# Kernel optimization log

Measured on AMD Instinct MI355X. Metric: run time of the kernel, lower is better.

## Reference

```python
import jax, jax.numpy as jnp
import numpy as np

EPS = 1e-3  # Keras BatchNormalization default epsilon
K = 7

def _bn(x, gamma, beta, mean, var):
    return gamma * (x - mean) * jax.lax.rsqrt(var + EPS) + beta

def setup_inputs() -> dict:
    key = jax.random.key(0)
    ks = jax.random.split(key, 4)
    B, L, Cin, F = 64, 512, 64, 128
    out_len = L - K + 1
    return {
        "x": jax.random.normal(ks[0], (B, L, Cin), jnp.float32),
        "conv_w": jax.random.normal(ks[1], (K, Cin, F), jnp.float32) * (1.0 / np.sqrt(K * Cin)),
        "conv_b": jnp.zeros((F,), jnp.float32),
        "bn1_gamma": jnp.ones((F,), jnp.float32),
        "bn1_beta": jnp.zeros((F,), jnp.float32),
        "bn1_mean": jnp.zeros((F,), jnp.float32),
        "bn1_var": jnp.ones((F,), jnp.float32),
        "local_w": jax.random.normal(ks[2], (out_len, K * F, F), jnp.float32) * (1.0 / np.sqrt(K * F)),
        "local_b": jnp.zeros((out_len, F), jnp.float32),
        "bn2_gamma": jnp.ones((F,), jnp.float32),
        "bn2_beta": jnp.zeros((F,), jnp.float32),
        "bn2_mean": jnp.zeros((F,), jnp.float32),
        "bn2_var": jnp.ones((F,), jnp.float32),
    }

def reference(x, conv_w, conv_b, bn1_gamma, bn1_beta, bn1_mean, bn1_var,
              local_w, local_b, bn2_gamma, bn2_beta, bn2_mean, bn2_var):
    # Conv1D, padding='same'  (NWC / WIO)
    y = jax.lax.conv_general_dilated(
        x, conv_w, window_strides=(1,), padding="SAME",
        dimension_numbers=("NWC", "WIO", "NWC")) + conv_b
    y = jax.nn.relu(_bn(y, bn1_gamma, bn1_beta, bn1_mean, bn1_var))

    # LocallyConnected1D, padding='valid': per-position unshared weights
    B, L, F = y.shape
    out_len = L - K + 1
    idx = jnp.arange(out_len)[:, None] + jnp.arange(K)[None, :]  # (out_len, K)
    patches = y[:, idx, :].reshape(B, out_len, K * F)             # (B, out_len, K*F)
    z = jnp.einsum("blk,lkf->blf", patches, local_w) + local_b    # (B, out_len, F)
    z = jax.nn.relu(_bn(z, bn2_gamma, bn2_beta, bn2_mean, bn2_var))
    return z
```

## Files before the change

### kernel.cpp

```cpp
#include <hip/hip_runtime.h>
#include <hip/hip_bf16.h>

typedef __attribute__((ext_vector_type(8))) short bf16x8;
typedef __attribute__((ext_vector_type(4))) float f32x4;

#define BB   64
#define LL   512
#define CIN  64
#define FF   128
#define KW   7
#define OUTL 506
#define LPAD 518
#define KC   448
#define KL   896
#define EPSV 1e-3f

static __device__ __forceinline__ short f2bf(float f) {
    unsigned u = __builtin_bit_cast(unsigned, f);
    unsigned r = (u + 0x7fffu + ((u >> 16) & 1u)) >> 16;
    return (short)r;
}

__global__ void pad_cvt_kernel(const float* __restrict__ x, short* __restrict__ xp) {
    int i = blockIdx.x * 256 + threadIdx.x;
    if (i >= BB * LPAD * CIN) return;
    int c  = i & (CIN - 1);
    int t  = i >> 6;
    int lp = t % LPAD;
    int b  = t / LPAD;
    float v = 0.0f;
    int l = lp - 3;
    if (l >= 0 && l < LL) v = x[(b * LL + l) * CIN + c];
    xp[i] = f2bf(v);
}

__global__ __launch_bounds__(256) void conv_bn_kernel(
    const short* __restrict__ xp, const float* __restrict__ w,
    const float* __restrict__ cb, const float* __restrict__ g,
    const float* __restrict__ be, const float* __restrict__ mu,
    const float* __restrict__ va, short* __restrict__ y) {
    const int lane = threadIdx.x & 63;
    const int wid  = threadIdx.x >> 6;
    const int m0   = blockIdx.x * 64;
    const int nb   = wid * 32;
    const int q    = lane >> 4;
    const int ln   = lane & 15;

    const short* arow[4];
#pragma unroll
    for (int mt = 0; mt < 4; ++mt) {
        int m = m0 + mt * 16 + ln;
        int b = m >> 9, l = m & 511;
        arow[mt] = xp + (b * LPAD + l) * CIN;
    }

    f32x4 acc[4][2];
#pragma unroll
    for (int mt = 0; mt < 4; ++mt)
#pragma unroll
        for (int nt = 0; nt < 2; ++nt) acc[mt][nt] = (f32x4){0.f, 0.f, 0.f, 0.f};

#pragma unroll 2
    for (int kc = 0; kc < KC; kc += 32) {
        const int ko = kc + q * 8;
        bf16x8 a[4];
#pragma unroll
        for (int mt = 0; mt < 4; ++mt)
            a[mt] = *(const bf16x8*)(arow[mt] + ko);
        bf16x8 bf[2];
#pragma unroll
        for (int nt = 0; nt < 2; ++nt) {
            const int n = nb + nt * 16 + ln;
            const float* wp = w + (size_t)ko * FF + n;
#pragma unroll
            for (int j = 0; j < 8; ++j) bf[nt][j] = f2bf(wp[(size_t)j * FF]);
        }
#pragma unroll
        for (int mt = 0; mt < 4; ++mt)
#pragma unroll
            for (int nt = 0; nt < 2; ++nt)
                acc[mt][nt] = __builtin_amdgcn_mfma_f32_16x16x32_bf16(
                    a[mt], bf[nt], acc[mt][nt], 0, 0, 0);
    }

#pragma unroll
    for (int nt = 0; nt < 2; ++nt) {
        const int n = nb + nt * 16 + ln;
        const float s  = g[n] * rsqrtf(va[n] + EPSV);
        const float b2 = s * (cb[n] - mu[n]) + be[n];
#pragma unroll
        for (int mt = 0; mt < 4; ++mt) {
            const int mbase = m0 + mt * 16 + q * 4;
#pragma unroll
            for (int r = 0; r < 4; ++r) {
                float v = fmaxf(acc[mt][nt][r] * s + b2, 0.0f);
                y[(size_t)(mbase + r) * FF + n] = f2bf(v);
            }
        }
    }
}

__global__ __launch_bounds__(256) void local_bn_kernel(
    const short* __restrict__ y, const float* __restrict__ lw,
    const float* __restrict__ lb, const float* __restrict__ g,
    const float* __restrict__ be, const float* __restrict__ mu,
    const float* __restrict__ va, float* __restrict__ out) {
    const int l    = blockIdx.x;
    const int lane = threadIdx.x & 63;
    const int wid  = threadIdx.x >> 6;
    const int nb   = wid * 32;
    const int q    = lane >> 4;
    const int ln   = lane & 15;

    const short* arow[4];
#pragma unroll
    for (int mt = 0; mt < 4; ++mt) {
        const int b = mt * 16 + ln;
        arow[mt] = y + (size_t)b * (LL * FF) + (size_t)l * FF;
    }
    const float* wl = lw + (size_t)l * (KL * FF);

    f32x4 acc[4][2];
#pragma unroll
    for (int mt = 0; mt < 4; ++mt)
#pragma unroll
        for (int nt = 0; nt < 2; ++nt) acc[mt][nt] = (f32x4){0.f, 0.f, 0.f, 0.f};

#pragma unroll 2
    for (int kc = 0; kc < KL; kc += 32) {
        const int ko = kc + q * 8;
        bf16x8 a[4];
#pragma unroll
        for (int mt = 0; mt < 4; ++mt)
            a[mt] = *(const bf16x8*)(arow[mt] + ko);
        bf16x8 bf[2];
#pragma unroll
        for (int nt = 0; nt < 2; ++nt) {
            const int n = nb + nt * 16 + ln;
            const float* wp = wl + (size_t)ko * FF + n;
#pragma unroll
            for (int j = 0; j < 8; ++j) bf[nt][j] = f2bf(wp[(size_t)j * FF]);
        }
#pragma unroll
        for (int mt = 0; mt < 4; ++mt)
#pragma unroll
            for (int nt = 0; nt < 2; ++nt)
                acc[mt][nt] = __builtin_amdgcn_mfma_f32_16x16x32_bf16(
                    a[mt], bf[nt], acc[mt][nt], 0, 0, 0);
    }

#pragma unroll
    for (int nt = 0; nt < 2; ++nt) {
        const int n = nb + nt * 16 + ln;
        const float s  = g[n] * rsqrtf(va[n] + EPSV);
        const float b2 = s * (lb[(size_t)l * FF + n] - mu[n]) + be[n];
#pragma unroll
        for (int mt = 0; mt < 4; ++mt) {
            const int bbase = mt * 16 + q * 4;
#pragma unroll
            for (int r = 0; r < 4; ++r) {
                float v = fmaxf(acc[mt][nt][r] * s + b2, 0.0f);
                out[(size_t)(bbase + r) * (OUTL * FF) + (size_t)l * FF + n] = v;
            }
        }
    }
}

extern "C" void kernel_launch(void* const* d_in, const int* in_sizes, int n_in,
                              void* d_out, int out_size, void* d_ws, size_t ws_size,
                              hipStream_t stream) {
    const float* x       = (const float*)d_in[0];
    const float* conv_w  = (const float*)d_in[1];
    const float* conv_b  = (const float*)d_in[2];
    const float* bn1_g   = (const float*)d_in[3];
    const float* bn1_b   = (const float*)d_in[4];
    const float* bn1_m   = (const float*)d_in[5];
    const float* bn1_v   = (const float*)d_in[6];
    const float* local_w = (const float*)d_in[7];
    const float* local_b = (const float*)d_in[8];
    const float* bn2_g   = (const float*)d_in[9];
    const float* bn2_b   = (const float*)d_in[10];
    const float* bn2_m   = (const float*)d_in[11];
    const float* bn2_v   = (const float*)d_in[12];
    float* out = (float*)d_out;

    short* xp  = (short*)d_ws;
    short* ybf = xp + (size_t)BB * LPAD * CIN;

    const int npad = BB * LPAD * CIN;
    pad_cvt_kernel<<<(npad + 255) / 256, 256, 0, stream>>>(x, xp);
    conv_bn_kernel<<<(BB * LL) / 64, 256, 0, stream>>>(
        xp, conv_w, conv_b, bn1_g, bn1_b, bn1_m, bn1_v, ybf);
    local_bn_kernel<<<OUTL, 256, 0, stream>>>(
        ybf, local_w, local_b, bn2_g, bn2_b, bn2_m, bn2_v, out);
}
```

Before: 379.4 us.

## Pre-transpose conv weights to bf16 and stage local weights through double-buffered LDS

The prep kernel now also converts the conv weights to bf16 in an N-major layout, so the conv kernel loads B fragments as single 16-byte vectors instead of eight strided fp32 loads each. The locally connected kernel streams each position's fp32 weight chunk into a double-buffered LDS tile with direct global-to-LDS loads, overlapping the next chunk's fetch with the current chunk's MFMAs. Fragments are then gathered from LDS with strided reads and converted to bf16. This adds one barrier per chunk, 32KB of LDS per block, and extra workspace for the transposed weights.

```diff
diff --git a/kernel.cpp b/kernel.cpp
--- a/kernel.cpp
+++ b/kernel.cpp
@@ -13,7 +13,14 @@
 #define LPAD 518
 #define KC   448
 #define KL   896
+#define BK   32
+#define NCH  28
 #define EPSV 1e-3f
+
+#define NPAD  (BB * LPAD * CIN)
+#define PADB  (NPAD / 256)
+#define NWT   (FF * KC)
+#define WTB   (NWT / 256)
 
 static __device__ __forceinline__ short f2bf(float f) {
     unsigned u = __builtin_bit_cast(unsigned, f);
@@ -21,21 +28,34 @@
     return (short)r;
 }
 
-__global__ void pad_cvt_kernel(const float* __restrict__ x, short* __restrict__ xp) {
-    int i = blockIdx.x * 256 + threadIdx.x;
-    if (i >= BB * LPAD * CIN) return;
-    int c  = i & (CIN - 1);
-    int t  = i >> 6;
-    int lp = t % LPAD;
-    int b  = t / LPAD;
-    float v = 0.0f;
-    int l = lp - 3;
-    if (l >= 0 && l < LL) v = x[(b * LL + l) * CIN + c];
-    xp[i] = f2bf(v);
+static __device__ __forceinline__ void g2lds16(const float* g, float* l) {
+    __builtin_amdgcn_global_load_lds(
+        (const __attribute__((address_space(1))) unsigned int*)g,
+        (__attribute__((address_space(3))) unsigned int*)l, 16, 0, 0);
+}
+
+__global__ void prep_kernel(const float* __restrict__ x, const float* __restrict__ w,
+                            short* __restrict__ xp, short* __restrict__ wt) {
+    if (blockIdx.x < PADB) {
+        int i = blockIdx.x * 256 + threadIdx.x;
+        int c  = i & (CIN - 1);
+        int t  = i >> 6;
+        int lp = t % LPAD;
+        int b  = t / LPAD;
+        float v = 0.0f;
+        int l = lp - 3;
+        if (l >= 0 && l < LL) v = x[(b * LL + l) * CIN + c];
+        xp[i] = f2bf(v);
+    } else {
+        int i = (blockIdx.x - PADB) * 256 + threadIdx.x;
+        int n = i / KC;
+        int k = i - n * KC;
+        wt[i] = f2bf(w[(size_t)k * FF + n]);
+    }
 }
 
 __global__ __launch_bounds__(256) void conv_bn_kernel(
-    const short* __restrict__ xp, const float* __restrict__ w,
+    const short* __restrict__ xp, const short* __restrict__ wt,
     const float* __restrict__ cb, const float* __restrict__ g,
     const float* __restrict__ be, const float* __restrict__ mu,
     const float* __restrict__ va, short* __restrict__ y) {
@@ -53,6 +73,10 @@
         int b = m >> 9, l = m & 511;
         arow[mt] = xp + (b * LPAD + l) * CIN;
     }
+    const short* brow[2];
+#pragma unroll
+    for (int nt = 0; nt < 2; ++nt)
+        brow[nt] = wt + (size_t)(nb + nt * 16 + ln) * KC;
 
     f32x4 acc[4][2];
 #pragma unroll
@@ -63,18 +87,11 @@
 #pragma unroll 2
     for (int kc = 0; kc < KC; kc += 32) {
         const int ko = kc + q * 8;
-        bf16x8 a[4];
-#pragma unroll
-        for (int mt = 0; mt < 4; ++mt)
-            a[mt] = *(const bf16x8*)(arow[mt] + ko);
-        bf16x8 bf[2];
-#pragma unroll
-        for (int nt = 0; nt < 2; ++nt) {
-            const int n = nb + nt * 16 + ln;
-            const float* wp = w + (size_t)ko * FF + n;
-#pragma unroll
-            for (int j = 0; j < 8; ++j) bf[nt][j] = f2bf(wp[(size_t)j * FF]);
-        }
+        bf16x8 a[4], bf[2];
+#pragma unroll
+        for (int mt = 0; mt < 4; ++mt) a[mt] = *(const bf16x8*)(arow[mt] + ko);
+#pragma unroll
+        for (int nt = 0; nt < 2; ++nt) bf[nt] = *(const bf16x8*)(brow[nt] + ko);
 #pragma unroll
         for (int mt = 0; mt < 4; ++mt)
 #pragma unroll
@@ -105,6 +122,7 @@
     const float* __restrict__ lb, const float* __restrict__ g,
     const float* __restrict__ be, const float* __restrict__ mu,
     const float* __restrict__ va, float* __restrict__ out) {
+    __shared__ float wtile[2][BK * FF];
     const int l    = blockIdx.x;
     const int lane = threadIdx.x & 63;
     const int wid  = threadIdx.x >> 6;
@@ -112,13 +130,12 @@
     const int q    = lane >> 4;
     const int ln   = lane & 15;
 
+    const float* wl = lw + (size_t)l * (KL * FF);
+
     const short* arow[4];
 #pragma unroll
-    for (int mt = 0; mt < 4; ++mt) {
-        const int b = mt * 16 + ln;
-        arow[mt] = y + (size_t)b * (LL * FF) + (size_t)l * FF;
-    }
-    const float* wl = lw + (size_t)l * (KL * FF);
+    for (int mt = 0; mt < 4; ++mt)
+        arow[mt] = y + (size_t)(mt * 16 + ln) * (LL * FF) + (size_t)l * FF;
 
     f32x4 acc[4][2];
 #pragma unroll
@@ -126,20 +143,38 @@
 #pragma unroll
         for (int nt = 0; nt < 2; ++nt) acc[mt][nt] = (f32x4){0.f, 0.f, 0.f, 0.f};
 
-#pragma unroll 2
-    for (int kc = 0; kc < KL; kc += 32) {
-        const int ko = kc + q * 8;
+    {
+        const float* src = wl;
+#pragma unroll
+        for (int r = 0; r < 4; ++r)
+            g2lds16(src + (size_t)(r * 256 + wid * 64 + lane) * 4,
+                    &wtile[0][(r * 256 + wid * 64) * 4]);
+    }
+
+    for (int c = 0; c < NCH; ++c) {
+        __syncthreads();
+        if (c + 1 < NCH) {
+            const float* src = wl + (size_t)(c + 1) * (BK * FF);
+            float* dst = wtile[(c + 1) & 1];
+#pragma unroll
+            for (int r = 0; r < 4; ++r)
+                g2lds16(src + (size_t)(r * 256 + wid * 64 + lane) * 4,
+                        &dst[(r * 256 + wid * 64) * 4]);
+        }
+        const float* wb = wtile[c & 1];
+        const int ko = c * BK + q * 8;
+
         bf16x8 a[4];
 #pragma unroll
-        for (int mt = 0; mt < 4; ++mt)
-            a[mt] = *(const bf16x8*)(arow[mt] + ko);
+        for (int mt = 0; mt < 4; ++mt) a[mt] = *(const bf16x8*)(arow[mt] + ko);
+
         bf16x8 bf[2];
 #pragma unroll
         for (int nt = 0; nt < 2; ++nt) {
             const int n = nb + nt * 16 + ln;
-            const float* wp = wl + (size_t)ko * FF + n;
-#pragma unroll
-            for (int j = 0; j < 8; ++j) bf[nt][j] = f2bf(wp[(size_t)j * FF]);
+#pragma unroll
+            for (int j = 0; j < 8; ++j)
+                bf[nt][j] = f2bf(wb[(q * 8 + j) * FF + n]);
         }
 #pragma unroll
         for (int mt = 0; mt < 4; ++mt)
@@ -185,12 +220,12 @@
     float* out = (float*)d_out;
 
     short* xp  = (short*)d_ws;
-    short* ybf = xp + (size_t)BB * LPAD * CIN;
-
-    const int npad = BB * LPAD * CIN;
-    pad_cvt_kernel<<<(npad + 255) / 256, 256, 0, stream>>>(x, xp);
+    short* ybf = xp + (size_t)NPAD;
+    short* wt  = ybf + (size_t)BB * LL * FF;
+
+    prep_kernel<<<PADB + WTB, 256, 0, stream>>>(x, conv_w, xp, wt);
     conv_bn_kernel<<<(BB * LL) / 64, 256, 0, stream>>>(
-        xp, conv_w, conv_b, bn1_g, bn1_b, bn1_m, bn1_v, ybf);
+        xp, wt, conv_b, bn1_g, bn1_b, bn1_m, bn1_v, ybf);
     local_bn_kernel<<<OUTL, 256, 0, stream>>>(
         ybf, local_w, local_b, bn2_g, bn2_b, bn2_m, bn2_v, out);
 }
```

Measured after the change: 374.8 us. About the same (-1.2%).
